# Performance work log

Measured on AMD Instinct MI355X. Metric: run time of the kernel, lower is better.

The kernel has to match this reference:

```python
import jax, jax.numpy as jnp
import numpy as np

B, N, D = 4, 2048, 1024
THRESHOLD_FACTOR = 1.25


def setup_inputs() -> dict:
    key = jax.random.key(0)
    ks = jax.random.split(key, 8)
    s = 0.02  # init scale matching torch.randn * 0.02
    return {
        "hidden_states": jax.random.normal(ks[0], (B, N, D), jnp.float32),
        "Wq": jax.random.normal(ks[1], (D, D), jnp.float32) * s,
        "bq": jnp.zeros((D,), jnp.float32),
        "Wk": jax.random.normal(ks[2], (D, D), jnp.float32) * s,
        "bk": jnp.zeros((D,), jnp.float32),
        "Wv": jax.random.normal(ks[3], (D, D), jnp.float32) * s,
        "bv": jnp.zeros((D,), jnp.float32),
        "Wo": jax.random.normal(ks[4], (D, D), jnp.float32) * s,
        "bo": jnp.zeros((D,), jnp.float32),
        "Wtq": jax.random.normal(ks[5], (2, D), jnp.float32) * s,  # nn.Linear(D, 2)
        "btq": jnp.zeros((2,), jnp.float32),
        "Wfq": jax.random.normal(ks[6], (D, 2), jnp.float32) * s,  # HebbianLinear(2, D)
        "bfq": jnp.zeros((D,), jnp.float32),
    }


def _linear(x, W, b):
    return x @ W.T + b


def reference(hidden_states, Wq, bq, Wk, bk, Wv, bv, Wo, bo, Wtq, btq, Wfq, bfq):
    d = hidden_states.shape[-1]
    q = _linear(hidden_states, Wq, bq)
    k = _linear(hidden_states, Wk, bk)
    v = _linear(hidden_states, Wv, bv)
    scores = jnp.einsum('bid,bjd->bij', q, k) / jnp.sqrt(jnp.asarray(d, scores_dtype := q.dtype))

    # PhaseAwareBinaryAttention on 2-d quantum projection
    qp = _linear(hidden_states, Wtq, btq)            # [B, N, 2]
    diff = qp[:, :, None, :] - qp[:, None, :, :]      # [B, N, N, 2]
    dist_sq = jnp.sum(diff * diff, axis=-1)           # [B, N, N]
    phase_diff = jnp.arctan2(diff[..., 1], diff[..., 0])
    forward_bias = 0.5 * (1.0 + jnp.cos(phase_diff))
    mean_dist = jnp.mean(dist_sq, axis=(-1, -2), keepdims=True)
    std_dist = jnp.std(dist_sq, axis=(-1, -2), keepdims=True, ddof=1)  # torch unbiased std
    threshold = mean_dist + THRESHOLD_FACTOR * std_dist
    n = dist_sq.shape[-1]
    causal = jnp.tril(jnp.ones((n, n), bool))
    valid = (dist_sq <= threshold) & causal[None]
    binary_attn = valid.astype(scores.dtype) * forward_bias

    masked = jnp.where(binary_attn == 0, -jnp.inf, scores)
    weights = jax.nn.softmax(masked, axis=-1)
    context = jnp.einsum('bij,bjd->bid', weights, v)
    output = _linear(context, Wo, bo)

    # F.normalize(qp, p=2, dim=-1) with eps=1e-12
    r_embed = qp / jnp.maximum(jnp.linalg.norm(qp, axis=-1, keepdims=True), 1e-12)
    quantum_output = _linear(r_embed, Wfq, bfq)
    return hidden_states + output + 0.1 * quantum_output
```

## Files before the change

kernel.cpp:

```cpp
#include <hip/hip_runtime.h>
#include <math.h>

#define N_TOK 2048
#define DIM   1024
#define BATCH 4

typedef float v4f  __attribute__((ext_vector_type(4)));
typedef __bf16 v8bf __attribute__((ext_vector_type(8)));
typedef unsigned short v8us __attribute__((ext_vector_type(8)));

static __device__ __forceinline__ unsigned short f2bf(float f) {
  unsigned int u = __float_as_uint(f);
  u += 0x7fffu + ((u >> 16) & 1u);
  return (unsigned short)(u >> 16);
}
static __device__ __forceinline__ float bf2f(unsigned short h) {
  return __uint_as_float((unsigned int)h << 16);
}

__global__ __launch_bounds__(256) void prep_kernel(
    const float* __restrict__ hs, const float* __restrict__ Wtq,
    const float* __restrict__ btq, unsigned short* __restrict__ hs_b,
    float2* __restrict__ qp, float2* __restrict__ remb,
    const float* __restrict__ W0, const float* __restrict__ W1,
    const float* __restrict__ W2, const float* __restrict__ W3,
    unsigned short* __restrict__ D0, unsigned short* __restrict__ D1,
    unsigned short* __restrict__ D2, unsigned short* __restrict__ D3) {
  int bx = blockIdx.x;
  if (bx < 2048) {
    int w = threadIdx.x >> 6, lane = threadIdx.x & 63;
    int row = bx * 4 + w;
    const float* x = hs + (size_t)row * DIM;
    unsigned short* d = hs_b + (size_t)row * DIM;
    float a0 = 0.f, a1 = 0.f;
#pragma unroll
    for (int it = 0; it < 4; ++it) {
      int base = it * 256 + lane * 4;
      float4 v = *(const float4*)(x + base);
      float4 w0 = *(const float4*)(Wtq + base);
      float4 w1 = *(const float4*)(Wtq + DIM + base);
      ushort4 pk;
      pk.x = f2bf(v.x); pk.y = f2bf(v.y); pk.z = f2bf(v.z); pk.w = f2bf(v.w);
      *(ushort4*)(d + base) = pk;
      a0 += v.x * w0.x + v.y * w0.y + v.z * w0.z + v.w * w0.w;
      a1 += v.x * w1.x + v.y * w1.y + v.z * w1.z + v.w * w1.w;
    }
    for (int o = 32; o; o >>= 1) { a0 += __shfl_xor(a0, o); a1 += __shfl_xor(a1, o); }
    if (lane == 0) {
      a0 += btq[0]; a1 += btq[1];
      qp[row] = make_float2(a0, a1);
      float nrm = fmaxf(sqrtf(a0 * a0 + a1 * a1), 1e-12f);
      remb[row] = make_float2(a0 / nrm, a1 / nrm);
    }
  } else {
    int idx = bx - 2048;
    int mat = idx >> 10, blk = idx & 1023;
    const float* s;
    unsigned short* d;
    switch (mat) {
      case 0: s = W0; d = D0; break;
      case 1: s = W1; d = D1; break;
      case 2: s = W2; d = D2; break;
      default: s = W3; d = D3; break;
    }
    int i = (blk * 256 + threadIdx.x) * 4;
    float4 v = *(const float4*)(s + i);
    d[i + 0] = f2bf(v.x); d[i + 1] = f2bf(v.y);
    d[i + 2] = f2bf(v.z); d[i + 3] = f2bf(v.w);
  }
}

__global__ __launch_bounds__(256) void moments_kernel(
    const float2* __restrict__ qp, double* __restrict__ part) {
  int b = blockIdx.y;
  int i0 = blockIdx.x * 32;
  const float2* qb = qp + ((size_t)b << 11);
  double s1 = 0.0, s2 = 0.0;
  for (int idx = threadIdx.x; idx < 32 * N_TOK; idx += 256) {
    int i = i0 + (idx >> 11), j = idx & (N_TOK - 1);
    float2 pi = qb[i], pj = qb[j];
    float dx = pi.x - pj.x, dy = pi.y - pj.y;
    float dd = __fadd_rn(__fmul_rn(dx, dx), __fmul_rn(dy, dy));
    s1 += (double)dd;
    s2 += (double)dd * (double)dd;
  }
  int lane = threadIdx.x & 63, w = threadIdx.x >> 6;
  for (int o = 32; o; o >>= 1) { s1 += __shfl_xor(s1, o); s2 += __shfl_xor(s2, o); }
  __shared__ double red[8];
  if (lane == 0) { red[w] = s1; red[4 + w] = s2; }
  __syncthreads();
  if (threadIdx.x == 0) {
    int slot = b * 64 + blockIdx.x;
    part[slot * 2 + 0] = red[0] + red[1] + red[2] + red[3];
    part[slot * 2 + 1] = red[4] + red[5] + red[6] + red[7];
  }
}

__global__ __launch_bounds__(256) void thr_kernel(
    const double* __restrict__ part, float* __restrict__ thr) {
  int b = threadIdx.x >> 6, lane = threadIdx.x & 63;
  double s1 = part[(b * 64 + lane) * 2 + 0];
  double s2 = part[(b * 64 + lane) * 2 + 1];
  for (int o = 32; o; o >>= 1) { s1 += __shfl_xor(s1, o); s2 += __shfl_xor(s2, o); }
  if (lane == 0) {
    double n2 = (double)N_TOK * (double)N_TOK;
    double mean = s1 / n2;
    double var = (s2 - n2 * mean * mean) / (n2 - 1.0);
    if (var < 0.0) var = 0.0;
    thr[b] = (float)(mean + 1.25 * sqrt(var));
  }
}

template<int NFRAG>
__device__ __forceinline__ void gemm_ktile_loopN(
    const unsigned short* __restrict__ Ag, const unsigned short* __restrict__ Bg,
    int ldA, int ldB, int kEnd,
    unsigned short* As, unsigned short* Bs, v4f acc[4][NFRAG]) {
  const int tid  = threadIdx.x;
  const int lane = tid & 63;
  const int wm   = ((tid >> 6) & 1) << 6;
  const int wn   = (tid >> 7) * (NFRAG * 16);
  const int quad = lane >> 4, l16 = lane & 15;
  const int srow = tid >> 3;
  const int scol = ((tid ^ srow) & 7) * 8;
  for (int k0 = 0; k0 < kEnd; k0 += 64) {
    __syncthreads();
#pragma unroll
    for (int it = 0; it < 4; ++it) {
      const unsigned short* ga = Ag + (size_t)(srow + it * 32) * ldA + k0 + scol;
      unsigned short* la = As + (size_t)(it * 256 + (tid & ~63)) * 8;
      __builtin_amdgcn_global_load_lds((const __attribute__((address_space(1))) void*)ga,
                                       (__attribute__((address_space(3))) void*)la, 16, 0, 0);
    }
#pragma unroll
    for (int it = 0; it < NFRAG; ++it) {
      const unsigned short* gb = Bg + (size_t)(srow + it * 32) * ldB + k0 + scol;
      unsigned short* lb = Bs + (size_t)(it * 256 + (tid & ~63)) * 8;
      __builtin_amdgcn_global_load_lds((const __attribute__((address_space(1))) void*)gb,
                                       (__attribute__((address_space(3))) void*)lb, 16, 0, 0);
    }
    asm volatile("s_waitcnt vmcnt(0)" ::: "memory");
    __syncthreads();
#pragma unroll
    for (int kk = 0; kk < 64; kk += 32) {
      const int co = ((((kk >> 3) + quad) ^ (l16 & 7)) << 3);
      v8bf af[4], bfv[NFRAG];
#pragma unroll
      for (int i = 0; i < 4; ++i)
        af[i] = *(const v8bf*)(As + (wm + i * 16 + l16) * 64 + co);
#pragma unroll
      for (int i = 0; i < NFRAG; ++i)
        bfv[i] = *(const v8bf*)(Bs + (wn + i * 16 + l16) * 64 + co);
#pragma unroll
      for (int mi = 0; mi < 4; ++mi)
#pragma unroll
        for (int ni = 0; ni < NFRAG; ++ni)
          acc[mi][ni] = __builtin_amdgcn_mfma_f32_16x16x32_bf16(af[mi], bfv[ni], acc[mi][ni], 0, 0, 0);
    }
  }
}

#define SBAR asm volatile("s_barrier" ::: "memory")

__device__ __forceinline__ void compute_12864(
    const unsigned short* As, const unsigned short* Bs,
    int wm, int wn, int quad, int l16, v4f acc[4][2]) {
#pragma unroll
  for (int kk = 0; kk < 64; kk += 32) {
    const int co = ((((kk >> 3) + quad) ^ (l16 & 7)) << 3);
    v8bf af[4], bfv[2];
#pragma unroll
    for (int i = 0; i < 4; ++i)
      af[i] = *(const v8bf*)(As + (wm + i * 16 + l16) * 64 + co);
#pragma unroll
    for (int i = 0; i < 2; ++i)
      bfv[i] = *(const v8bf*)(Bs + (wn + i * 16 + l16) * 64 + co);
    __builtin_amdgcn_s_setprio(1);
#pragma unroll
    for (int mi = 0; mi < 4; ++mi)
#pragma unroll
      for (int ni = 0; ni < 2; ++ni)
        acc[mi][ni] = __builtin_amdgcn_mfma_f32_16x16x32_bf16(af[mi], bfv[ni], acc[mi][ni], 0, 0, 0);
    __builtin_amdgcn_s_setprio(0);
  }
}

__device__ __forceinline__ void gemm_ktile_loop64_cnt(
    const unsigned short* __restrict__ Ag, const unsigned short* __restrict__ Bg,
    int ldA, int ldB, int kEnd,
    unsigned short* As0, unsigned short* Bs0,
    unsigned short* As1, unsigned short* Bs1, v4f acc[4][2]) {
  const int tid  = threadIdx.x;
  const int lane = tid & 63;
  const int wm   = ((tid >> 6) & 1) << 6;
  const int wn   = (tid >> 7) << 5;
  const int quad = lane >> 4, l16 = lane & 15;
  const int srow = tid >> 3;
  const int scol = ((tid ^ srow) & 7) * 8;
  const unsigned short* gA = Ag + (size_t)srow * ldA + scol;
  const unsigned short* gB = Bg + (size_t)srow * ldB + scol;
  const int lbase = (tid & ~63) * 8;

  auto stage = [&](unsigned short* As, unsigned short* Bs, int k0) {
#pragma unroll
    for (int it = 0; it < 4; ++it) {
      const unsigned short* ga = gA + (size_t)(it * 32) * ldA + k0;
      __builtin_amdgcn_global_load_lds((const __attribute__((address_space(1))) void*)ga,
                                       (__attribute__((address_space(3))) void*)(As + it * 2048 + lbase), 16, 0, 0);
    }
#pragma unroll
    for (int it = 0; it < 2; ++it) {
      const unsigned short* gb = gB + (size_t)(it * 32) * ldB + k0;
      __builtin_amdgcn_global_load_lds((const __attribute__((address_space(1))) void*)gb,
                                       (__attribute__((address_space(3))) void*)(Bs + it * 2048 + lbase), 16, 0, 0);
    }
  };

  stage(As0, Bs0, 0);
  stage(As1, Bs1, 64);
  int k0 = 0;
  for (; k0 + 128 < kEnd; k0 += 128) {
    asm volatile("s_waitcnt vmcnt(6)" ::: "memory");
    SBAR;
    compute_12864(As0, Bs0, wm, wn, quad, l16, acc);
    SBAR;
    stage(As0, Bs0, k0 + 128);
    asm volatile("s_waitcnt vmcnt(6)" ::: "memory");
    SBAR;
    compute_12864(As1, Bs1, wm, wn, quad, l16, acc);
    SBAR;
    stage(As1, Bs1, k0 + 192);
  }
  asm volatile("s_waitcnt vmcnt(6)" ::: "memory");
  SBAR;
  compute_12864(As0, Bs0, wm, wn, quad, l16, acc);
  SBAR;
  asm volatile("s_waitcnt vmcnt(0)" ::: "memory");
  SBAR;
  compute_12864(As1, Bs1, wm, wn, quad, l16, acc);
}

#define PROLOG128                                                     \
  __shared__ __attribute__((aligned(16))) unsigned short smem[2][128 * 64];\
  unsigned short* As = smem[0];                                       \
  unsigned short* Bs = smem[1];                                       \
  v4f acc[4][4];                                                      \
  _Pragma("unroll") for (int i_ = 0; i_ < 4; ++i_)                    \
  _Pragma("unroll") for (int j_ = 0; j_ < 4; ++j_)                    \
      acc[i_][j_] = v4f{0.f, 0.f, 0.f, 0.f};                          \
  const int lane = threadIdx.x & 63, w = threadIdx.x >> 6;            \
  const int wm = (w & 1) << 6, wn = (w >> 1) << 6;                    \
  const int quad = lane >> 4, l16 = lane & 15;

#define PROLOG12864DB                                                 \
  __shared__ __attribute__((aligned(16))) unsigned short Asm[2][128 * 64];\
  __shared__ __attribute__((aligned(16))) unsigned short Bsm[2][64 * 64]; \
  v4f acc[4][2];                                                      \
  _Pragma("unroll") for (int i_ = 0; i_ < 4; ++i_)                    \
  _Pragma("unroll") for (int j_ = 0; j_ < 2; ++j_)                    \
      acc[i_][j_] = v4f{0.f, 0.f, 0.f, 0.f};                          \
  const int lane = threadIdx.x & 63, w = threadIdx.x >> 6;            \
  const int wm = (w & 1) << 6, wn = (w >> 1) << 5;                    \
  const int quad = lane >> 4, l16 = lane & 15;

__global__ __launch_bounds__(256) void gemm_qkv_fused_kernel(
    const unsigned short* __restrict__ X, const unsigned short* __restrict__ Wqkv,
    const float* __restrict__ bq, const float* __restrict__ bk,
    const float* __restrict__ bv, unsigned short* __restrict__ q_b,
    unsigned short* __restrict__ k_b, unsigned short* __restrict__ v_t) {
  PROLOG128
  int lid = blockIdx.y * 24 + blockIdx.x;
  int xcd = lid & 7, slot = lid >> 3;
  int by = (xcd << 3) | (slot & 7);
  int bx = slot >> 3;
  int m0 = by * 128, n0 = bx * 128;
  gemm_ktile_loopN<4>(X + (size_t)m0 * DIM, Wqkv + (size_t)n0 * DIM, DIM, DIM, DIM, As, Bs, acc);
  int region = n0 >> 10;
  const float* bias = region == 0 ? bq : region == 1 ? bk : bv;
  int cbase = n0 & 1023;
  if (region < 2) {
    unsigned short* dst = region == 0 ? q_b : k_b;
#pragma unroll
    for (int mi = 0; mi < 4; ++mi) {
      int row0 = m0 + wm + mi * 16 + quad * 4;
#pragma unroll
      for (int ni = 0; ni < 4; ++ni) {
        int col = cbase + wn + ni * 16 + l16;
        float bcol = bias[col];
#pragma unroll
        for (int r = 0; r < 4; ++r)
          dst[(size_t)(row0 + r) * DIM + col] = f2bf(acc[mi][ni][r] + bcol);
      }
    }
  } else {
    unsigned short* T = &smem[0][0];
    __syncthreads();
#pragma unroll
    for (int mi = 0; mi < 4; ++mi) {
      int trow = wm + mi * 16 + quad * 4;
#pragma unroll
      for (int ni = 0; ni < 4; ++ni) {
        int fcol = wn + ni * 16 + l16;
        float bcol = bias[cbase + fcol];
        ushort4 pk;
        pk.x = f2bf(acc[mi][ni][0] + bcol);
        pk.y = f2bf(acc[mi][ni][1] + bcol);
        pk.z = f2bf(acc[mi][ni][2] + bcol);
        pk.w = f2bf(acc[mi][ni][3] + bcol);
        *(ushort4*)(T + fcol * 128 + (trow ^ ((fcol & 7) << 3))) = pk;
      }
    }
    __syncthreads();
    int bb = m0 >> 11, tok0 = m0 & (N_TOK - 1);
    unsigned short* dstb = v_t + ((size_t)(bb << 10) + cbase) * N_TOK + tok0;
#pragma unroll
    for (int kk2 = 0; kk2 < 8; ++kk2) {
      int c = kk2 * 256 + threadIdx.x;
      int f = c >> 4, e0 = (c & 15) * 8;
      v8us v = *(const v8us*)(T + f * 128 + (e0 ^ ((f & 7) << 3)));
      *(v8us*)(dstb + (size_t)f * N_TOK + e0) = v;
    }
  }
}

__global__ __launch_bounds__(256) void gemm_scores_kernel(
    const unsigned short* __restrict__ q, const unsigned short* __restrict__ k,
    const float2* __restrict__ qp, const float* __restrict__ thr,
    unsigned short* __restrict__ S) {
  PROLOG12864DB
  int b = blockIdx.y;
  int lid = blockIdx.x;
  int t = (lid & 7) * 34 + (lid >> 3);
  int ti = (int)((sqrtf(4.f * (float)t + 1.f) - 1.f) * 0.5f);
  while ((ti + 1) * (ti + 2) <= t) ++ti;
  while (ti * (ti + 1) > t) --ti;
  int tj = t - ti * (ti + 1);
  int i0 = ti * 128, j0 = tj * 64;
  const unsigned short* qb = q + (size_t)b * N_TOK * DIM;
  const unsigned short* kb = k + (size_t)b * N_TOK * DIM;
  gemm_ktile_loop64_cnt(qb + (size_t)i0 * DIM, kb + (size_t)j0 * DIM, DIM, DIM, DIM,
                        Asm[0], Bsm[0], Asm[1], Bsm[1], acc);
  float th = thr[b];
  const float2* qpb = qp + ((size_t)b << 11);
  unsigned short* Sb = S + (size_t)b * N_TOK * N_TOK;
  float2 pjv[2];
#pragma unroll
  for (int ni = 0; ni < 2; ++ni) pjv[ni] = qpb[j0 + wn + ni * 16 + l16];
#pragma unroll
  for (int mi = 0; mi < 4; ++mi) {
#pragma unroll
    for (int r = 0; r < 4; ++r) {
      int i = i0 + wm + mi * 16 + quad * 4 + r;
      float2 pi2 = qpb[i];
#pragma unroll
      for (int ni = 0; ni < 2; ++ni) {
        int j = j0 + wn + ni * 16 + l16;
        if (j <= i) {
          float dx = pi2.x - pjv[ni].x, dy = pi2.y - pjv[ni].y;
          float dd = __fadd_rn(__fmul_rn(dx, dx), __fmul_rn(dy, dy));
          bool ok = (dd <= th);
          if (ok && dx < 0.f && fabsf(dy) <= 3e-4f * (-dx)) {
            float fb = 0.5f * (1.f + cosf(atan2f(dy, dx)));
            if (fb == 0.f) ok = false;
          }
          Sb[(size_t)i * N_TOK + j] = ok ? f2bf(acc[mi][ni][r] * 0.03125f) : 0xFF80;
        }
      }
    }
  }
}

__global__ __launch_bounds__(256) void softmax_kernel(
    const unsigned short* __restrict__ S, unsigned short* __restrict__ P) {
  int row = blockIdx.x;
  int b = row >> 11, i = row & (N_TOK - 1);
  const unsigned short* s = S + ((size_t)b * N_TOK + i) * N_TOK;
  unsigned short* p = P + ((size_t)b * N_TOK + i) * N_TOK;
  int tid = threadIdx.x, lane = tid & 63, w = tid >> 6;
  int lim = i + 1;
  int tail0 = lim & ~7, ntail = lim - tail0;
  __shared__ float redmax[4], redsum[4];
  float mx = -__builtin_inff();
  for (int j = tid * 8; j + 8 <= lim; j += 2048) {
    v8us v = *(const v8us*)(s + j);
#pragma unroll
    for (int e = 0; e < 8; ++e) mx = fmaxf(mx, bf2f(v[e]));
  }
  if (tid < ntail) mx = fmaxf(mx, bf2f(s[tail0 + tid]));
  for (int o = 32; o; o >>= 1) mx = fmaxf(mx, __shfl_xor(mx, o));
  if (lane == 0) redmax[w] = mx;
  __syncthreads();
  mx = fmaxf(fmaxf(redmax[0], redmax[1]), fmaxf(redmax[2], redmax[3]));
  float sum = 0.f;
  for (int j = tid * 8; j + 8 <= lim; j += 2048) {
    v8us v = *(const v8us*)(s + j);
#pragma unroll
    for (int e = 0; e < 8; ++e) sum += __expf(bf2f(v[e]) - mx);
  }
  if (tid < ntail) sum += __expf(bf2f(s[tail0 + tid]) - mx);
  for (int o = 32; o; o >>= 1) sum += __shfl_xor(sum, o);
  if (lane == 0) redsum[w] = sum;
  __syncthreads();
  sum = redsum[0] + redsum[1] + redsum[2] + redsum[3];
  float inv = 1.f / sum;
  for (int j = tid * 8; j + 8 <= lim; j += 2048) {
    v8us v = *(const v8us*)(s + j);
    v8us o;
#pragma unroll
    for (int e = 0; e < 8; ++e) o[e] = f2bf(__expf(bf2f(v[e]) - mx) * inv);
    *(v8us*)(p + j) = o;
  }
  if (tid < ntail) p[tail0 + tid] = f2bf(__expf(bf2f(s[tail0 + tid]) - mx) * inv);
  int zs = (lim + 7) & ~7;
  if (tid < zs - lim) p[lim + tid] = 0;
  int rend = (lim + 127) & ~127;
  v8us zv;
#pragma unroll
  for (int e = 0; e < 8; ++e) zv[e] = 0;
  for (int j = zs + tid * 8; j < rend; j += 2048) *(v8us*)(p + j) = zv;
}

__global__ __launch_bounds__(256) void gemm_pv_kernel(
    const unsigned short* __restrict__ P, const unsigned short* __restrict__ vt,
    unsigned short* __restrict__ ctx) {
  PROLOG12864DB
  int b = blockIdx.z;
  int ti = 15 - blockIdx.y;
  int d0 = blockIdx.x * 64;
  int i0 = ti * 128;
  const unsigned short* Pb = P + (size_t)b * N_TOK * N_TOK;
  const unsigned short* Vb = vt + ((size_t)b * DIM + d0) * N_TOK;
  int kEnd = (ti + 1) * 128;
  gemm_ktile_loop64_cnt(Pb + (size_t)i0 * N_TOK, Vb, N_TOK, N_TOK, kEnd,
                        Asm[0], Bsm[0], Asm[1], Bsm[1], acc);
#pragma unroll
  for (int mi = 0; mi < 4; ++mi) {
    int row0 = i0 + wm + mi * 16 + quad * 4;
#pragma unroll
    for (int ni = 0; ni < 2; ++ni) {
      int d = d0 + wn + ni * 16 + l16;
#pragma unroll
      for (int r = 0; r < 4; ++r)
        ctx[((size_t)b * N_TOK + row0 + r) * DIM + d] = f2bf(acc[mi][ni][r]);
    }
  }
}

__global__ __launch_bounds__(256) void gemm_out_kernel(
    const unsigned short* __restrict__ ctx, const unsigned short* __restrict__ Wob,
    const float* __restrict__ bo, const float* __restrict__ hs,
    const float2* __restrict__ remb, const float* __restrict__ Wfq,
    const float* __restrict__ bfq, float* __restrict__ out) {
  PROLOG12864DB
  int lid = blockIdx.y * 16 + blockIdx.x;
  int xcd = lid & 7, slot = lid >> 3;
  int by = (xcd << 3) | (slot & 7);
  int bx = slot >> 3;
  int m0 = by * 128, n0 = bx * 64;
  gemm_ktile_loop64_cnt(ctx + (size_t)m0 * DIM, Wob + (size_t)n0 * DIM, DIM, DIM, DIM,
                        Asm[0], Bsm[0], Asm[1], Bsm[1], acc);
#pragma unroll
  for (int mi = 0; mi < 4; ++mi) {
    int row0 = m0 + wm + mi * 16 + quad * 4;
#pragma unroll
    for (int ni = 0; ni < 2; ++ni) {
      int col = n0 + wn + ni * 16 + l16;
      float bias2 = bo[col] + 0.1f * bfq[col];
      float wf0 = 0.1f * Wfq[col * 2 + 0], wf1 = 0.1f * Wfq[col * 2 + 1];
#pragma unroll
      for (int r = 0; r < 4; ++r) {
        int row = row0 + r;
        float2 re = remb[row];
        out[(size_t)row * DIM + col] =
            acc[mi][ni][r] + bias2 + hs[(size_t)row * DIM + col] + re.x * wf0 + re.y * wf1;
      }
    }
  }
}

extern "C" void kernel_launch(void* const* d_in, const int* in_sizes, int n_in,
                              void* d_out, int out_size, void* d_ws, size_t ws_size,
                              hipStream_t stream) {
  const float* hs  = (const float*)d_in[0];
  const float* Wq  = (const float*)d_in[1];
  const float* bq  = (const float*)d_in[2];
  const float* Wk  = (const float*)d_in[3];
  const float* bk  = (const float*)d_in[4];
  const float* Wv  = (const float*)d_in[5];
  const float* bv  = (const float*)d_in[6];
  const float* Wo  = (const float*)d_in[7];
  const float* bo  = (const float*)d_in[8];
  const float* Wtq = (const float*)d_in[9];
  const float* btq = (const float*)d_in[10];
  const float* Wfq = (const float*)d_in[11];
  const float* bfq = (const float*)d_in[12];
  float* out = (float*)d_out;

  char* ws = (char*)d_ws;
  size_t off = 0;
  auto alloc = [&](size_t bytes) {
    char* p = ws + off;
    off += (bytes + 255) & ~(size_t)255;
    return p;
  };
  unsigned short* hs_b = (unsigned short*)alloc((size_t)8192 * 1024 * 2);
  unsigned short* q_b  = (unsigned short*)alloc((size_t)8192 * 1024 * 2);
  unsigned short* k_b  = (unsigned short*)alloc((size_t)8192 * 1024 * 2);
  unsigned short* v_t  = (unsigned short*)alloc((size_t)8192 * 1024 * 2);
  unsigned short* Wq_b = (unsigned short*)alloc((size_t)1024 * 1024 * 2);
  unsigned short* Wk_b = (unsigned short*)alloc((size_t)1024 * 1024 * 2);
  unsigned short* Wv_b = (unsigned short*)alloc((size_t)1024 * 1024 * 2);
  unsigned short* Wo_b = (unsigned short*)alloc((size_t)1024 * 1024 * 2);
  float2* qp   = (float2*)alloc((size_t)8192 * 8);
  float2* remb = (float2*)alloc((size_t)8192 * 8);
  double* part = (double*)alloc((size_t)BATCH * 64 * 2 * 8);
  float*  thr  = (float*)alloc(64);
  unsigned short* S = (unsigned short*)alloc((size_t)BATCH * N_TOK * N_TOK * 2);
  unsigned short* P   = q_b;
  unsigned short* ctx = hs_b;

  prep_kernel<<<6144, 256, 0, stream>>>(hs, Wtq, btq, hs_b, qp, remb,
                                        Wq, Wk, Wv, Wo, Wq_b, Wk_b, Wv_b, Wo_b);
  moments_kernel<<<dim3(64, BATCH), 256, 0, stream>>>((const float2*)qp, part);
  thr_kernel<<<1, 256, 0, stream>>>(part, thr);

  gemm_qkv_fused_kernel<<<dim3(24, 64), 256, 0, stream>>>(
      hs_b, Wq_b, bq, bk, bv, q_b, k_b, v_t);

  gemm_scores_kernel<<<dim3(272, 4), 256, 0, stream>>>(
      q_b, k_b, (const float2*)qp, thr, S);

  softmax_kernel<<<8192, 256, 0, stream>>>(S, P);

  gemm_pv_kernel<<<dim3(16, 16, 4), 256, 0, stream>>>(P, v_t, ctx);

  gemm_out_kernel<<<dim3(16, 64), 256, 0, stream>>>(ctx, Wo_b, bo, hs, remb, Wfq, bfq, out);
}
```

Measured before the change: 340.7 us.

## Use 128x128 tiles with 512-thread blocks for PV and output GEMMs

Adds a new K-loop and compute routine that gives each block a 128x128 output tile computed by 8 waves, each owning a 64x32 sub-tile. Both the P·V GEMM and the output projection GEMM switch from 128x64 tiles with 256 threads to this scheme, halving the block count. The aim is more reuse of each staged LDS tile and less redundant global traffic for the A operand. In exchange, LDS per block grows and there are fewer blocks to spread over the CUs, which hurts tail balance and latency hiding, especially for the triangular PV grid.

```diff
diff --git a/kernel.cpp b/kernel.cpp
--- a/kernel.cpp
+++ b/kernel.cpp
@@ -240,6 +240,81 @@
   compute_12864(As1, Bs1, wm, wn, quad, l16, acc);
 }
 
+__device__ __forceinline__ void compute_128128w(
+    const unsigned short* As, const unsigned short* Bs,
+    int wm, int wn, int quad, int l16, v4f acc[4][2]) {
+#pragma unroll
+  for (int kk = 0; kk < 64; kk += 32) {
+    const int co = ((((kk >> 3) + quad) ^ (l16 & 7)) << 3);
+    v8bf af[4], bfv[2];
+#pragma unroll
+    for (int i = 0; i < 4; ++i)
+      af[i] = *(const v8bf*)(As + (wm + i * 16 + l16) * 64 + co);
+#pragma unroll
+    for (int i = 0; i < 2; ++i)
+      bfv[i] = *(const v8bf*)(Bs + (wn + i * 16 + l16) * 64 + co);
+    __builtin_amdgcn_s_setprio(1);
+#pragma unroll
+    for (int mi = 0; mi < 4; ++mi)
+#pragma unroll
+      for (int ni = 0; ni < 2; ++ni)
+        acc[mi][ni] = __builtin_amdgcn_mfma_f32_16x16x32_bf16(af[mi], bfv[ni], acc[mi][ni], 0, 0, 0);
+    __builtin_amdgcn_s_setprio(0);
+  }
+}
+
+__device__ __forceinline__ void gemm_ktile_loop128w_cnt(
+    const unsigned short* __restrict__ Ag, const unsigned short* __restrict__ Bg,
+    int ldA, int ldB, int kEnd,
+    unsigned short* As0, unsigned short* Bs0,
+    unsigned short* As1, unsigned short* Bs1, v4f acc[4][2],
+    int wm, int wn, int quad, int l16) {
+  const int tid  = threadIdx.x;
+  const int srow = tid >> 3;
+  const int scol = ((tid ^ srow) & 7) * 8;
+  const unsigned short* gA = Ag + (size_t)srow * ldA + scol;
+  const unsigned short* gB = Bg + (size_t)srow * ldB + scol;
+  const int lbase = (tid & ~63) * 8;
+
+  auto stage = [&](unsigned short* As, unsigned short* Bs, int k0) {
+#pragma unroll
+    for (int it = 0; it < 2; ++it) {
+      const unsigned short* ga = gA + (size_t)(it * 64) * ldA + k0;
+      __builtin_amdgcn_global_load_lds((const __attribute__((address_space(1))) void*)ga,
+                                       (__attribute__((address_space(3))) void*)(As + it * 4096 + lbase), 16, 0, 0);
+    }
+#pragma unroll
+    for (int it = 0; it < 2; ++it) {
+      const unsigned short* gb = gB + (size_t)(it * 64) * ldB + k0;
+      __builtin_amdgcn_global_load_lds((const __attribute__((address_space(1))) void*)gb,
+                                       (__attribute__((address_space(3))) void*)(Bs + it * 4096 + lbase), 16, 0, 0);
+    }
+  };
+
+  stage(As0, Bs0, 0);
+  stage(As1, Bs1, 64);
+  int k0 = 0;
+  for (; k0 + 128 < kEnd; k0 += 128) {
+    asm volatile("s_waitcnt vmcnt(4)" ::: "memory");
+    SBAR;
+    compute_128128w(As0, Bs0, wm, wn, quad, l16, acc);
+    SBAR;
+    stage(As0, Bs0, k0 + 128);
+    asm volatile("s_waitcnt vmcnt(4)" ::: "memory");
+    SBAR;
+    compute_128128w(As1, Bs1, wm, wn, quad, l16, acc);
+    SBAR;
+    stage(As1, Bs1, k0 + 192);
+  }
+  asm volatile("s_waitcnt vmcnt(4)" ::: "memory");
+  SBAR;
+  compute_128128w(As0, Bs0, wm, wn, quad, l16, acc);
+  SBAR;
+  asm volatile("s_waitcnt vmcnt(0)" ::: "memory");
+  SBAR;
+  compute_128128w(As1, Bs1, wm, wn, quad, l16, acc);
+}
+
 #define PROLOG128                                                     \
   __shared__ __attribute__((aligned(16))) unsigned short smem[2][128 * 64];\
   unsigned short* As = smem[0];                                       \
@@ -261,6 +336,17 @@
       acc[i_][j_] = v4f{0.f, 0.f, 0.f, 0.f};                          \
   const int lane = threadIdx.x & 63, w = threadIdx.x >> 6;            \
   const int wm = (w & 1) << 6, wn = (w >> 1) << 5;                    \
+  const int quad = lane >> 4, l16 = lane & 15;
+
+#define PROLOG128128W                                                 \
+  __shared__ __attribute__((aligned(16))) unsigned short Asm[2][128 * 64];\
+  __shared__ __attribute__((aligned(16))) unsigned short Bsm[2][128 * 64];\
+  v4f acc[4][2];                                                      \
+  _Pragma("unroll") for (int i_ = 0; i_ < 4; ++i_)                    \
+  _Pragma("unroll") for (int j_ = 0; j_ < 2; ++j_)                    \
+      acc[i_][j_] = v4f{0.f, 0.f, 0.f, 0.f};                          \
+  const int lane = threadIdx.x & 63, wid = threadIdx.x >> 6;          \
+  const int wm = (wid & 1) << 6, wn = (wid >> 1) << 5;                \
   const int quad = lane >> 4, l16 = lane & 15;
 
 __global__ __launch_bounds__(256) void gemm_qkv_fused_kernel(
@@ -420,19 +506,19 @@
   for (int j = zs + tid * 8; j < rend; j += 2048) *(v8us*)(p + j) = zv;
 }
 
-__global__ __launch_bounds__(256) void gemm_pv_kernel(
+__global__ __launch_bounds__(512, 4) void gemm_pv_kernel(
     const unsigned short* __restrict__ P, const unsigned short* __restrict__ vt,
     unsigned short* __restrict__ ctx) {
-  PROLOG12864DB
+  PROLOG128128W
   int b = blockIdx.z;
   int ti = 15 - blockIdx.y;
-  int d0 = blockIdx.x * 64;
+  int d0 = blockIdx.x * 128;
   int i0 = ti * 128;
   const unsigned short* Pb = P + (size_t)b * N_TOK * N_TOK;
   const unsigned short* Vb = vt + ((size_t)b * DIM + d0) * N_TOK;
   int kEnd = (ti + 1) * 128;
-  gemm_ktile_loop64_cnt(Pb + (size_t)i0 * N_TOK, Vb, N_TOK, N_TOK, kEnd,
-                        Asm[0], Bsm[0], Asm[1], Bsm[1], acc);
+  gemm_ktile_loop128w_cnt(Pb + (size_t)i0 * N_TOK, Vb, N_TOK, N_TOK, kEnd,
+                          Asm[0], Bsm[0], Asm[1], Bsm[1], acc, wm, wn, quad, l16);
 #pragma unroll
   for (int mi = 0; mi < 4; ++mi) {
     int row0 = i0 + wm + mi * 16 + quad * 4;
@@ -446,19 +532,19 @@
   }
 }
 
-__global__ __launch_bounds__(256) void gemm_out_kernel(
+__global__ __launch_bounds__(512, 4) void gemm_out_kernel(
     const unsigned short* __restrict__ ctx, const unsigned short* __restrict__ Wob,
     const float* __restrict__ bo, const float* __restrict__ hs,
     const float2* __restrict__ remb, const float* __restrict__ Wfq,
     const float* __restrict__ bfq, float* __restrict__ out) {
-  PROLOG12864DB
-  int lid = blockIdx.y * 16 + blockIdx.x;
+  PROLOG128128W
+  int lid = blockIdx.y * 8 + blockIdx.x;
   int xcd = lid & 7, slot = lid >> 3;
   int by = (xcd << 3) | (slot & 7);
   int bx = slot >> 3;
-  int m0 = by * 128, n0 = bx * 64;
-  gemm_ktile_loop64_cnt(ctx + (size_t)m0 * DIM, Wob + (size_t)n0 * DIM, DIM, DIM, DIM,
-                        Asm[0], Bsm[0], Asm[1], Bsm[1], acc);
+  int m0 = by * 128, n0 = bx * 128;
+  gemm_ktile_loop128w_cnt(ctx + (size_t)m0 * DIM, Wob + (size_t)n0 * DIM, DIM, DIM, DIM,
+                          Asm[0], Bsm[0], Asm[1], Bsm[1], acc, wm, wn, quad, l16);
 #pragma unroll
   for (int mi = 0; mi < 4; ++mi) {
     int row0 = m0 + wm + mi * 16 + quad * 4;
@@ -532,7 +618,7 @@
 
   softmax_kernel<<<8192, 256, 0, stream>>>(S, P);
 
-  gemm_pv_kernel<<<dim3(16, 16, 4), 256, 0, stream>>>(P, v_t, ctx);
-
-  gemm_out_kernel<<<dim3(16, 64), 256, 0, stream>>>(ctx, Wo_b, bo, hs, remb, Wfq, bfq, out);
-}
+  gemm_pv_kernel<<<dim3(8, 16, 4), 512, 0, stream>>>(P, v_t, ctx);
+
+  gemm_out_kernel<<<dim3(8, 64), 512, 0, stream>>>(ctx, Wo_b, bo, hs, remb, Wfq, bfq, out);
+}
```

New measurement: 330.1 us. 1.03x faster.

## Widen attention GEMM tiles to 128x128 with 8 waves and fold threshold into scores

Applied to the files above, without the earlier changes.

The scores, PV and output-projection GEMMs move from 128x64 tiles on 256 threads to 128x128 tiles on 512 threads. Each wave still computes a 64x32 sub-tile, and the global-to-LDS staging is re-indexed so each thread loads 64-row strides. The larger tile reuses each loaded A tile over twice as many columns, which roughly halves redundant global and L2 traffic and the number of blocks. The separate single-block threshold kernel is removed; each scores block now reduces the per-batch moments itself after its GEMM, saving one launch. In exchange, LDS use per block doubles, the grid has fewer blocks (136x4 for scores), and the triangular tiling is coarser, which may leave CUs idle or reduce occupancy.

```diff
diff --git a/kernel.cpp b/kernel.cpp
--- a/kernel.cpp
+++ b/kernel.cpp
@@ -96,21 +96,6 @@
   }
 }
 
-__global__ __launch_bounds__(256) void thr_kernel(
-    const double* __restrict__ part, float* __restrict__ thr) {
-  int b = threadIdx.x >> 6, lane = threadIdx.x & 63;
-  double s1 = part[(b * 64 + lane) * 2 + 0];
-  double s2 = part[(b * 64 + lane) * 2 + 1];
-  for (int o = 32; o; o >>= 1) { s1 += __shfl_xor(s1, o); s2 += __shfl_xor(s2, o); }
-  if (lane == 0) {
-    double n2 = (double)N_TOK * (double)N_TOK;
-    double mean = s1 / n2;
-    double var = (s2 - n2 * mean * mean) / (n2 - 1.0);
-    if (var < 0.0) var = 0.0;
-    thr[b] = (float)(mean + 1.25 * sqrt(var));
-  }
-}
-
 template<int NFRAG>
 __device__ __forceinline__ void gemm_ktile_loopN(
     const unsigned short* __restrict__ Ag, const unsigned short* __restrict__ Bg,
@@ -162,7 +147,7 @@
 
 #define SBAR asm volatile("s_barrier" ::: "memory")
 
-__device__ __forceinline__ void compute_12864(
+__device__ __forceinline__ void compute_128128w(
     const unsigned short* As, const unsigned short* Bs,
     int wm, int wn, int quad, int l16, v4f acc[4][2]) {
 #pragma unroll
@@ -185,16 +170,13 @@
   }
 }
 
-__device__ __forceinline__ void gemm_ktile_loop64_cnt(
+__device__ __forceinline__ void gemm_ktile_loop128w_cnt(
     const unsigned short* __restrict__ Ag, const unsigned short* __restrict__ Bg,
     int ldA, int ldB, int kEnd,
     unsigned short* As0, unsigned short* Bs0,
-    unsigned short* As1, unsigned short* Bs1, v4f acc[4][2]) {
+    unsigned short* As1, unsigned short* Bs1, v4f acc[4][2],
+    int wm, int wn, int quad, int l16) {
   const int tid  = threadIdx.x;
-  const int lane = tid & 63;
-  const int wm   = ((tid >> 6) & 1) << 6;
-  const int wn   = (tid >> 7) << 5;
-  const int quad = lane >> 4, l16 = lane & 15;
   const int srow = tid >> 3;
   const int scol = ((tid ^ srow) & 7) * 8;
   const unsigned short* gA = Ag + (size_t)srow * ldA + scol;
@@ -203,16 +185,16 @@
 
   auto stage = [&](unsigned short* As, unsigned short* Bs, int k0) {
 #pragma unroll
-    for (int it = 0; it < 4; ++it) {
-      const unsigned short* ga = gA + (size_t)(it * 32) * ldA + k0;
+    for (int it = 0; it < 2; ++it) {
+      const unsigned short* ga = gA + (size_t)(it * 64) * ldA + k0;
       __builtin_amdgcn_global_load_lds((const __attribute__((address_space(1))) void*)ga,
-                                       (__attribute__((address_space(3))) void*)(As + it * 2048 + lbase), 16, 0, 0);
+                                       (__attribute__((address_space(3))) void*)(As + it * 4096 + lbase), 16, 0, 0);
     }
 #pragma unroll
     for (int it = 0; it < 2; ++it) {
-      const unsigned short* gb = gB + (size_t)(it * 32) * ldB + k0;
+      const unsigned short* gb = gB + (size_t)(it * 64) * ldB + k0;
       __builtin_amdgcn_global_load_lds((const __attribute__((address_space(1))) void*)gb,
-                                       (__attribute__((address_space(3))) void*)(Bs + it * 2048 + lbase), 16, 0, 0);
+                                       (__attribute__((address_space(3))) void*)(Bs + it * 4096 + lbase), 16, 0, 0);
     }
   };
 
@@ -220,24 +202,24 @@
   stage(As1, Bs1, 64);
   int k0 = 0;
   for (; k0 + 128 < kEnd; k0 += 128) {
-    asm volatile("s_waitcnt vmcnt(6)" ::: "memory");
+    asm volatile("s_waitcnt vmcnt(4)" ::: "memory");
     SBAR;
-    compute_12864(As0, Bs0, wm, wn, quad, l16, acc);
+    compute_128128w(As0, Bs0, wm, wn, quad, l16, acc);
     SBAR;
     stage(As0, Bs0, k0 + 128);
-    asm volatile("s_waitcnt vmcnt(6)" ::: "memory");
+    asm volatile("s_waitcnt vmcnt(4)" ::: "memory");
     SBAR;
-    compute_12864(As1, Bs1, wm, wn, quad, l16, acc);
+    compute_128128w(As1, Bs1, wm, wn, quad, l16, acc);
     SBAR;
     stage(As1, Bs1, k0 + 192);
   }
-  asm volatile("s_waitcnt vmcnt(6)" ::: "memory");
+  asm volatile("s_waitcnt vmcnt(4)" ::: "memory");
   SBAR;
-  compute_12864(As0, Bs0, wm, wn, quad, l16, acc);
+  compute_128128w(As0, Bs0, wm, wn, quad, l16, acc);
   SBAR;
   asm volatile("s_waitcnt vmcnt(0)" ::: "memory");
   SBAR;
-  compute_12864(As1, Bs1, wm, wn, quad, l16, acc);
+  compute_128128w(As1, Bs1, wm, wn, quad, l16, acc);
 }
 
 #define PROLOG128                                                     \
@@ -252,15 +234,15 @@
   const int wm = (w & 1) << 6, wn = (w >> 1) << 6;                    \
   const int quad = lane >> 4, l16 = lane & 15;
 
-#define PROLOG12864DB                                                 \
+#define PROLOG128128W                                                 \
   __shared__ __attribute__((aligned(16))) unsigned short Asm[2][128 * 64];\
-  __shared__ __attribute__((aligned(16))) unsigned short Bsm[2][64 * 64]; \
+  __shared__ __attribute__((aligned(16))) unsigned short Bsm[2][128 * 64];\
   v4f acc[4][2];                                                      \
   _Pragma("unroll") for (int i_ = 0; i_ < 4; ++i_)                    \
   _Pragma("unroll") for (int j_ = 0; j_ < 2; ++j_)                    \
       acc[i_][j_] = v4f{0.f, 0.f, 0.f, 0.f};                          \
-  const int lane = threadIdx.x & 63, w = threadIdx.x >> 6;            \
-  const int wm = (w & 1) << 6, wn = (w >> 1) << 5;                    \
+  const int lane = threadIdx.x & 63, wid = threadIdx.x >> 6;          \
+  const int wm = (wid & 1) << 6, wn = (wid >> 1) << 5;                \
   const int quad = lane >> 4, l16 = lane & 15;
 
 __global__ __launch_bounds__(256) void gemm_qkv_fused_kernel(
@@ -323,24 +305,38 @@
   }
 }
 
-__global__ __launch_bounds__(256) void gemm_scores_kernel(
+__global__ __launch_bounds__(512, 4) void gemm_scores_kernel(
     const unsigned short* __restrict__ q, const unsigned short* __restrict__ k,
-    const float2* __restrict__ qp, const float* __restrict__ thr,
+    const float2* __restrict__ qp, const double* __restrict__ part,
     unsigned short* __restrict__ S) {
-  PROLOG12864DB
+  PROLOG128128W
+  __shared__ float thsh;
   int b = blockIdx.y;
   int lid = blockIdx.x;
-  int t = (lid & 7) * 34 + (lid >> 3);
-  int ti = (int)((sqrtf(4.f * (float)t + 1.f) - 1.f) * 0.5f);
-  while ((ti + 1) * (ti + 2) <= t) ++ti;
-  while (ti * (ti + 1) > t) --ti;
-  int tj = t - ti * (ti + 1);
-  int i0 = ti * 128, j0 = tj * 64;
+  int t = (lid & 7) * 17 + (lid >> 3);
+  int ti = (int)((sqrtf(8.f * (float)t + 1.f) - 1.f) * 0.5f);
+  while ((ti + 1) * (ti + 2) / 2 <= t) ++ti;
+  while (ti * (ti + 1) / 2 > t) --ti;
+  int tj = t - ti * (ti + 1) / 2;
+  int i0 = ti * 128, j0 = tj * 128;
   const unsigned short* qb = q + (size_t)b * N_TOK * DIM;
   const unsigned short* kb = k + (size_t)b * N_TOK * DIM;
-  gemm_ktile_loop64_cnt(qb + (size_t)i0 * DIM, kb + (size_t)j0 * DIM, DIM, DIM, DIM,
-                        Asm[0], Bsm[0], Asm[1], Bsm[1], acc);
-  float th = thr[b];
+  gemm_ktile_loop128w_cnt(qb + (size_t)i0 * DIM, kb + (size_t)j0 * DIM, DIM, DIM, DIM,
+                          Asm[0], Bsm[0], Asm[1], Bsm[1], acc, wm, wn, quad, l16);
+  if (threadIdx.x < 64) {
+    double s1 = part[(b * 64 + lane) * 2 + 0];
+    double s2 = part[(b * 64 + lane) * 2 + 1];
+    for (int o = 32; o; o >>= 1) { s1 += __shfl_xor(s1, o); s2 += __shfl_xor(s2, o); }
+    if (lane == 0) {
+      double n2 = (double)N_TOK * (double)N_TOK;
+      double mean = s1 / n2;
+      double var = (s2 - n2 * mean * mean) / (n2 - 1.0);
+      if (var < 0.0) var = 0.0;
+      thsh = (float)(mean + 1.25 * sqrt(var));
+    }
+  }
+  __syncthreads();
+  float th = thsh;
   const float2* qpb = qp + ((size_t)b << 11);
   unsigned short* Sb = S + (size_t)b * N_TOK * N_TOK;
   float2 pjv[2];
@@ -420,19 +416,19 @@
   for (int j = zs + tid * 8; j < rend; j += 2048) *(v8us*)(p + j) = zv;
 }
 
-__global__ __launch_bounds__(256) void gemm_pv_kernel(
+__global__ __launch_bounds__(512, 4) void gemm_pv_kernel(
     const unsigned short* __restrict__ P, const unsigned short* __restrict__ vt,
     unsigned short* __restrict__ ctx) {
-  PROLOG12864DB
+  PROLOG128128W
   int b = blockIdx.z;
   int ti = 15 - blockIdx.y;
-  int d0 = blockIdx.x * 64;
+  int d0 = blockIdx.x * 128;
   int i0 = ti * 128;
   const unsigned short* Pb = P + (size_t)b * N_TOK * N_TOK;
   const unsigned short* Vb = vt + ((size_t)b * DIM + d0) * N_TOK;
   int kEnd = (ti + 1) * 128;
-  gemm_ktile_loop64_cnt(Pb + (size_t)i0 * N_TOK, Vb, N_TOK, N_TOK, kEnd,
-                        Asm[0], Bsm[0], Asm[1], Bsm[1], acc);
+  gemm_ktile_loop128w_cnt(Pb + (size_t)i0 * N_TOK, Vb, N_TOK, N_TOK, kEnd,
+                          Asm[0], Bsm[0], Asm[1], Bsm[1], acc, wm, wn, quad, l16);
 #pragma unroll
   for (int mi = 0; mi < 4; ++mi) {
     int row0 = i0 + wm + mi * 16 + quad * 4;
@@ -446,19 +442,19 @@
   }
 }
 
-__global__ __launch_bounds__(256) void gemm_out_kernel(
+__global__ __launch_bounds__(512, 4) void gemm_out_kernel(
     const unsigned short* __restrict__ ctx, const unsigned short* __restrict__ Wob,
     const float* __restrict__ bo, const float* __restrict__ hs,
     const float2* __restrict__ remb, const float* __restrict__ Wfq,
     const float* __restrict__ bfq, float* __restrict__ out) {
-  PROLOG12864DB
-  int lid = blockIdx.y * 16 + blockIdx.x;
+  PROLOG128128W
+  int lid = blockIdx.y * 8 + blockIdx.x;
   int xcd = lid & 7, slot = lid >> 3;
   int by = (xcd << 3) | (slot & 7);
   int bx = slot >> 3;
-  int m0 = by * 128, n0 = bx * 64;
-  gemm_ktile_loop64_cnt(ctx + (size_t)m0 * DIM, Wob + (size_t)n0 * DIM, DIM, DIM, DIM,
-                        Asm[0], Bsm[0], Asm[1], Bsm[1], acc);
+  int m0 = by * 128, n0 = bx * 128;
+  gemm_ktile_loop128w_cnt(ctx + (size_t)m0 * DIM, Wob + (size_t)n0 * DIM, DIM, DIM, DIM,
+                          Asm[0], Bsm[0], Asm[1], Bsm[1], acc, wm, wn, quad, l16);
 #pragma unroll
   for (int mi = 0; mi < 4; ++mi) {
     int row0 = m0 + wm + mi * 16 + quad * 4;
@@ -518,21 +514,21 @@
   unsigned short* S = (unsigned short*)alloc((size_t)BATCH * N_TOK * N_TOK * 2);
   unsigned short* P   = q_b;
   unsigned short* ctx = hs_b;
+  (void)thr;
 
   prep_kernel<<<6144, 256, 0, stream>>>(hs, Wtq, btq, hs_b, qp, remb,
                                         Wq, Wk, Wv, Wo, Wq_b, Wk_b, Wv_b, Wo_b);
   moments_kernel<<<dim3(64, BATCH), 256, 0, stream>>>((const float2*)qp, part);
-  thr_kernel<<<1, 256, 0, stream>>>(part, thr);
 
   gemm_qkv_fused_kernel<<<dim3(24, 64), 256, 0, stream>>>(
       hs_b, Wq_b, bq, bk, bv, q_b, k_b, v_t);
 
-  gemm_scores_kernel<<<dim3(272, 4), 256, 0, stream>>>(
-      q_b, k_b, (const float2*)qp, thr, S);
+  gemm_scores_kernel<<<dim3(136, 4), 512, 0, stream>>>(
+      q_b, k_b, (const float2*)qp, (const double*)part, S);
 
   softmax_kernel<<<8192, 256, 0, stream>>>(S, P);
 
-  gemm_pv_kernel<<<dim3(16, 16, 4), 256, 0, stream>>>(P, v_t, ctx);
-
-  gemm_out_kernel<<<dim3(16, 64), 256, 0, stream>>>(ctx, Wo_b, bo, hs, remb, Wfq, bfq, out);
-}
+  gemm_pv_kernel<<<dim3(8, 16, 4), 512, 0, stream>>>(P, v_t, ctx);
+
+  gemm_out_kernel<<<dim3(8, 64), 512, 0, stream>>>(ctx, Wo_b, bo, hs, remb, Wfq, bfq, out);
+}
```

Measured after the change: 333.7 us. 1.02x faster.
